# Optimization experiments

Hardware: AMD Instinct MI355X
Metric: run time of the kernel (lower is better)

The kernel has to match this reference:

```python
import jax, jax.numpy as jnp
import numpy as np
from jax import lax

B, T, D, H = 64, 256, 512, 1024  # batch, n_seq(time), seq_len(feat), hidden_dim

def _lstm(xs, h0, c0, W, U, b):
    # xs: (T, B, in_dim); W: (in_dim, 4H); U: (H, 4H); gate order i,f,g,o
    def step(carry, xt):
        h, c = carry
        gates = xt @ W + h @ U + b  # (B, 4H)
        i, f, g, o = jnp.split(gates, 4, axis=-1)
        c = jax.nn.sigmoid(f) * c + jax.nn.sigmoid(i) * jnp.tanh(g)
        h = jax.nn.sigmoid(o) * jnp.tanh(c)
        return (h, c), h
    (hT, cT), ys = lax.scan(step, (h0, c0), xs)
    return ys, (hT, cT)

def setup_inputs() -> dict:
    key = jax.random.key(0)
    ks = jax.random.split(key, 20)
    s = 0.02
    inp = {
        "x": jax.random.normal(ks[0], (B, T, D), jnp.float32),
        "h0": jax.random.normal(ks[1], (B, H), jnp.float32) * 0.1,
        "c0": jax.random.normal(ks[2], (B, H), jnp.float32) * 0.1,
        "W1": jax.random.normal(ks[3], (D, 4 * H), jnp.float32) * s,
        "U1": jax.random.normal(ks[4], (H, 4 * H), jnp.float32) * s,
        "b1": jnp.zeros((4 * H,), jnp.float32),
        "W2": jax.random.normal(ks[5], (H, 4 * H), jnp.float32) * s,
        "U2": jax.random.normal(ks[6], (H, 4 * H), jnp.float32) * s,
        "b2": jnp.zeros((4 * H,), jnp.float32),
        "fc1_w": jax.random.normal(ks[7], (H, H // 2), jnp.float32) * s,
        "fc1_b": jnp.zeros((H // 2,), jnp.float32),
        "fc2_w": jax.random.normal(ks[8], (H // 2 * T, 36), jnp.float32) * s,
        "fc2_b": jnp.zeros((36,), jnp.float32),
        "fc3_w": jax.random.normal(ks[9], (36, 6), jnp.float32) * s,
        "fc3_b": jnp.zeros((6,), jnp.float32),
        "fc4_w": jax.random.normal(ks[10], (6, 6), jnp.float32) * s,
        "fc4_b": jnp.zeros((6,), jnp.float32),
    }
    return inp

def reference(x, h0, c0, W1, U1, b1, W2, U2, b2,
              fc1_w, fc1_b, fc2_w, fc2_b, fc3_w, fc3_b, fc4_w, fc4_b):
    xs = jnp.transpose(x, (1, 0, 2))           # (T, B, D)
    ys1, (h1, c1) = _lstm(xs, h0, c0, W1, U1, b1)
    ys2, _ = _lstm(ys1, h1, c1, W2, U2, b2)    # lstm2 seeded with lstm1 final states
    y = jnp.transpose(ys2, (1, 0, 2))          # (B, T, H)
    y = y @ fc1_w + fc1_b                      # (B, T, H/2)
    y = y.reshape(y.shape[0], -1)              # (B, T*H/2)
    y = y @ fc2_w + fc2_b
    y = y @ fc3_w + fc3_b
    y = y @ fc4_w + fc4_b
    return jax.nn.relu(y)
```

## Files before the change

kernel.cpp:

```cpp
#include <hip/hip_runtime.h>


#define NT 256

typedef _Float16 f16x8 __attribute__((ext_vector_type(8)));
typedef _Float16 f16x4 __attribute__((ext_vector_type(4)));
typedef float f32x4 __attribute__((ext_vector_type(4)));
typedef unsigned long long u64;

__device__ __forceinline__ float sigm(float x)   { return 1.0f / (1.0f + __expf(-x)); }
__device__ __forceinline__ float tanh_f(float x) { return 1.0f - 2.0f / (__expf(2.0f * x) + 1.0f); }

__device__ __forceinline__ void barrier_lds() {
  asm volatile("s_waitcnt lgkmcnt(0)" ::: "memory");
  __builtin_amdgcn_s_barrier();
  asm volatile("" ::: "memory");
}


__global__ void prep_x_kernel(const float* __restrict__ x, _Float16* __restrict__ xh) {
  int id = blockIdx.x * blockDim.x + threadIdx.x;
  int j = id & 7, b = (id >> 3) & 63, cg = (id >> 9) & 63, t = id >> 15;
  xh[id] = (_Float16)x[((size_t)b * 256 + t) * 512 + cg * 8 + j];
}

__global__ void swizzle_b_kernel(const float* __restrict__ src0, const float* __restrict__ src1,
                                 int k0, int K, int N, int srcStride, int permute,
                                 _Float16* __restrict__ dst) {
  int id = blockIdx.x * blockDim.x + threadIdx.x;
  int total = (N / 16) * (K / 32) * 64;
  if (id >= total) return;
  int lane = id & 63;
  int kb = (id >> 6) % (K / 32);
  int nt = id / ((K / 32) * 64);
  int kbase = kb * 32 + ((lane >> 4) << 3);
  int pc = nt * 16 + (lane & 15);
  int oc = permute ? ((pc & 3) * 1024 + (pc >> 2)) : pc;
  f16x8 v;
  #pragma unroll
  for (int j = 0; j < 8; ++j) {
    int k = kbase + j;
    float f = (k < k0) ? src0[(size_t)k * srcStride + oc]
                       : src1[(size_t)(k - k0) * srcStride + oc];
    v[j] = (_Float16)f;
  }
  ((f16x8*)dst)[id] = v;
}

__global__ void prep_small_kernel(const float* __restrict__ b1, const float* __restrict__ b2,
                                  const float* __restrict__ h0,
                                  float* __restrict__ b1p, float* __restrict__ b2p,
                                  _Float16* __restrict__ ys1_0, int* __restrict__ bar) {
  int i = blockIdx.x * blockDim.x + threadIdx.x;
  if (i < 4096) {
    int oc = (i & 3) * 1024 + (i >> 2);
    b1p[i] = b1[oc];
    b2p[i] = b2[oc];
  }
  if (i < 65536) {
    int j = i & 7, b = (i >> 3) & 63, cg = i >> 9;
    ys1_0[i] = (_Float16)h0[b * 1024 + cg * 8 + j];
  }
  if (i < 16384) bar[i] = 0;
}

__global__ void sentinel_fill_kernel(_Float16* __restrict__ ys1, _Float16* __restrict__ ys2) {
  size_t i = (size_t)blockIdx.x * blockDim.x + threadIdx.x;
  uint4 s = {0x7FFF7FFFu, 0x7FFF7FFFu, 0x7FFF7FFFu, 0x7FFF7FFFu};
  ((uint4*)(ys1 + 65536))[i] = s;
  ((uint4*)(ys2 + 65536))[i] = s;
}

__launch_bounds__(256, 2)
__global__ void xg_gemm_kernel(const _Float16* __restrict__ xsrc, size_t xts, int kxb,
                               const _Float16* __restrict__ bfrag, const float* __restrict__ biasp,
                               _Float16* __restrict__ xg) {
  __shared__ _Float16 Bs[2 * 32 * 64 * 8];
  const int tid = threadIdx.x;
  const int lane = tid & 63;
  const int w = tid >> 6;
  const int btc = blockIdx.x >> 8;
  const int gb = blockIdx.x & 255;
  const int mb = gb & 1, nb = gb >> 1;
  const int KB = kxb + 32;
  if (tid == 0)
    (void)__hip_atomic_load((const int*)biasp, __ATOMIC_ACQUIRE, __HIP_MEMORY_SCOPE_AGENT);
  __syncthreads();
  #pragma unroll
  for (int h = 0; h < 2; ++h) {
    const uint4* s = (const uint4*)bfrag + (size_t)((2 * nb + h) * KB) * 64;
    uint4* d = (uint4*)Bs + h * 2048;
    for (int i = tid; i < kxb * 64; i += NT) d[i] = s[i];
  }
  __syncthreads();
  const f16x8* Bv = (const f16x8*)Bs;
  const int q = lane >> 4;
  const float bias0 = biasp[(2 * nb + 0) * 16 + (lane & 15)];
  const float bias1 = biasp[(2 * nb + 1) * 16 + (lane & 15)];
  for (int i = 0; i < 32; ++i) {
    int t = btc * 128 + i * 4 + w;
    const f16x8* ax = (const f16x8*)(xsrc + (size_t)t * xts);
    f32x4 acc[4];
    acc[0] = (f32x4){bias0, bias0, bias0, bias0};
    acc[1] = (f32x4){bias0, bias0, bias0, bias0};
    acc[2] = (f32x4){bias1, bias1, bias1, bias1};
    acc[3] = (f32x4){bias1, bias1, bias1, bias1};
    #pragma unroll 8
    for (int kb = 0; kb < kxb; ++kb) {
      f16x8 a0 = ax[(kb * 4 + q) * 64 + mb * 32 + (lane & 15)];
      f16x8 a1 = ax[(kb * 4 + q) * 64 + mb * 32 + 16 + (lane & 15)];
      f16x8 b0 = Bv[kb * 64 + lane];
      f16x8 b1v = Bv[2048 + kb * 64 + lane];
      acc[0] = __builtin_amdgcn_mfma_f32_16x16x32_f16(a0, b0, acc[0], 0, 0, 0);
      acc[1] = __builtin_amdgcn_mfma_f32_16x16x32_f16(a1, b0, acc[1], 0, 0, 0);
      acc[2] = __builtin_amdgcn_mfma_f32_16x16x32_f16(a0, b1v, acc[2], 0, 0, 0);
      acc[3] = __builtin_amdgcn_mfma_f32_16x16x32_f16(a1, b1v, acc[3], 0, 0, 0);
    }
    #pragma unroll
    for (int wp = 0; wp < 4; ++wp) {
      f16x4 hv;
      #pragma unroll
      for (int j = 0; j < 4; ++j) hv[j] = (_Float16)acc[wp][j];
      ((f16x4*)xg)[((size_t)t * 256 + gb) * 256 + wp * 64 + lane] = hv;
    }
  }
}

__launch_bounds__(NT, 1)
__global__ void lstm_layer_kernel(const _Float16* __restrict__ xg,
                                  _Float16* hseq, const _Float16* __restrict__ hinit,
                                  const _Float16* __restrict__ bfrag, int kxb,
                                  const float* __restrict__ cin, float* __restrict__ cout,
                                  int* bar) {
  __shared__ _Float16 Bs[2 * 32 * 64 * 8];
  __shared__ _Float16 As[128 * 32 * 8];
  __shared__ __align__(16) float gt[4][16 * 20];
  __shared__ u64 hl[4][16];
  const int tid = threadIdx.x;
  const int lane = tid & 63;
  const int w = tid >> 6;
  const int wm = w & 1, wn = w >> 1;
  const int blk = blockIdx.x;
  const int mb = blk & 1, nb = blk >> 1;
  const int KB = kxb + 32;

  if (tid == 0)
    (void)__hip_atomic_load(&bar[1024], __ATOMIC_ACQUIRE, __HIP_MEMORY_SCOPE_AGENT);
  __syncthreads();

  #pragma unroll
  for (int h = 0; h < 2; ++h) {
    const uint4* s = (const uint4*)bfrag + (size_t)((2 * nb + h) * KB + kxb) * 64;
    uint4* d = (uint4*)Bs + h * 2048;
    for (int i = tid; i < 2048; i += NT) d[i] = s[i];
  }
  __syncthreads();

  const f16x8* Bv = (const f16x8*)Bs;
  const f16x8* Af = (const f16x8*)As;
  u64* As64 = (u64*)As;
  const int q = lane >> 4;
  const int lrow = wm * 16 + (lane & 15);
  float cc = cin[(size_t)(mb * 32 + wm * 16 + (lane >> 2)) * 1024 + nb * 8 + wn * 4 + (lane & 3)];
  float* gw = &gt[w][0];
  _Float16* hw = (_Float16*)&hl[w][0];
  const u64 hstIdx = (u64)(nb * 128 + (mb * 32 + wm * 16 + (lane & 15)) * 2 + wn);
  int* fbase = bar + mb * 4096;
  const int* fpoll = fbase + (size_t)(w * 32 + (lane & 31)) * 32;
  int* fown = fbase + nb * 32;

  for (int t = 0; t < 256; ++t) {
    f16x4 xgv = ((const f16x4*)xg)[((size_t)t * 256 + blk) * 256 + w * 64 + lane];
    if (t) {
      for (;;) {
        int v = __hip_atomic_load(fpoll, __ATOMIC_RELAXED, __HIP_MEMORY_SCOPE_AGENT);
        if (__all(v >= t)) break;
        __builtin_amdgcn_s_sleep(1);
      }
      asm volatile("" ::: "memory");
    }
    const u64* hp = (const u64*)((t == 0) ? hinit : (hseq + (size_t)t * 65536))
                  + (size_t)(w * 32) * 128 + mb * 64 + lane;
    u64 hvv[32];
    #pragma unroll
    for (int i = 0; i < 32; ++i)
      hvv[i] = __hip_atomic_load(hp + (size_t)i * 128, __ATOMIC_RELAXED, __HIP_MEMORY_SCOPE_AGENT);
    for (;;) {
      unsigned np = 0;
      #pragma unroll
      for (int i = 0; i < 32; ++i)
        np |= (((unsigned)hvv[i] == 0x7FFF7FFFu) ? 1u : 0u) << i;
      if (__all(np == 0)) break;
      __builtin_amdgcn_s_sleep(1);
      #pragma unroll
      for (int i = 0; i < 32; ++i)
        if ((np >> i) & 1)
          hvv[i] = __hip_atomic_load(hp + (size_t)i * 128, __ATOMIC_RELAXED, __HIP_MEMORY_SCOPE_AGENT);
    }
    #pragma unroll
    for (int i = 0; i < 32; ++i) As64[(w * 32 + i) * 64 + lane] = hvv[i];
    barrier_lds();
    f32x4 acc = {(float)xgv[0], (float)xgv[1], (float)xgv[2], (float)xgv[3]};
    f32x4 acc2 = {0.f, 0.f, 0.f, 0.f};
    #pragma unroll 8
    for (int kb = 0; kb < 16; ++kb) {
      acc  = __builtin_amdgcn_mfma_f32_16x16x32_f16(Af[((2 * kb) * 4 + q) * 32 + lrow],
                                                    Bv[(wn * 32 + 2 * kb) * 64 + lane], acc, 0, 0, 0);
      acc2 = __builtin_amdgcn_mfma_f32_16x16x32_f16(Af[((2 * kb + 1) * 4 + q) * 32 + lrow],
                                                    Bv[(wn * 32 + 2 * kb + 1) * 64 + lane], acc2, 0, 0, 0);
    }
    #pragma unroll
    for (int r = 0; r < 4; ++r) acc[r] += acc2[r];
    #pragma unroll
    for (int r = 0; r < 4; ++r) gw[(q * 4 + r) * 20 + (lane & 15)] = acc[r];
    float4 gv = *(float4*)&gw[(lane >> 2) * 20 + (lane & 3) * 4];
    cc = sigm(gv.y) * cc + sigm(gv.x) * tanh_f(gv.z);
    float hn = sigm(gv.w) * tanh_f(cc);
    hw[lane] = (_Float16)hn;
    u64 hv = hl[w][lane & 15];
    if (lane < 16)
      __hip_atomic_store((u64*)(hseq + (size_t)(t + 1) * 65536) + hstIdx, hv,
                         __ATOMIC_RELAXED, __HIP_MEMORY_SCOPE_AGENT);
    barrier_lds();
    if (t < 255 && tid == 0)
      __hip_atomic_store(fown, t + 1, __ATOMIC_RELAXED, __HIP_MEMORY_SCOPE_AGENT);
  }
  if (cout)
    cout[(size_t)(mb * 32 + wm * 16 + (lane >> 2)) * 1024 + nb * 8 + wn * 4 + (lane & 3)] = cc;
}


__launch_bounds__(256, 1)
__global__ void fc1_gemm_kernel(const _Float16* __restrict__ ys2, const _Float16* __restrict__ wfrag,
                                const float* __restrict__ fc1b, float* __restrict__ Y1) {
  const int mb = blockIdx.x >> 3;
  const int nb = blockIdx.x & 7;
  const int tid = threadIdx.x;
  const int lane = tid & 63;
  const int w = tid >> 6;
  const int q = lane >> 4;
  const int R0 = mb * 64 + w * 16;
  const int arow = R0 + (lane & 15);
  const int u = arow >> 6;
  const int b = arow & 63;
  const f16x8* A = (const f16x8*)(ys2 + (size_t)(u + 1) * 65536);
  const f16x8* W = (const f16x8*)wfrag;
  f32x4 acc[4];
  #pragma unroll
  for (int n = 0; n < 4; ++n) acc[n] = (f32x4){0.f, 0.f, 0.f, 0.f};
  #pragma unroll 4
  for (int kb = 0; kb < 32; ++kb) {
    f16x8 a = A[(kb * 4 + q) * 64 + b];
    #pragma unroll
    for (int n = 0; n < 4; ++n)
      acc[n] = __builtin_amdgcn_mfma_f32_16x16x32_f16(a, W[(((nb * 4 + n) * 32) + kb) * 64 + lane],
                                                      acc[n], 0, 0, 0);
  }
  const int rb = R0 + (q << 2);
  #pragma unroll
  for (int n = 0; n < 4; ++n) {
    int col = nb * 64 + n * 16 + (lane & 15);
    float bias = fc1b[col];
    #pragma unroll
    for (int r = 0; r < 4; ++r) {
      int R = rb + r;
      Y1[((size_t)(R & 63) * 256 + (R >> 6)) * 512 + col] = acc[n][r] + bias;
    }
  }
}

__global__ void fc2_partial_kernel(const float* __restrict__ Y1, const float* __restrict__ fc2w,
                                   float* __restrict__ part) {
  int kc = blockIdx.x;
  int tid = threadIdx.x;
  int b = tid >> 2, qq = tid & 3;
  const float* y = Y1 + (size_t)b * 131072 + (size_t)kc * 512;
  const float* wbase = fc2w + (size_t)kc * 512 * 36 + qq * 9;
  float acc[9];
  #pragma unroll
  for (int j = 0; j < 9; ++j) acc[j] = 0.f;
  for (int k = 0; k < 512; ++k) {
    float yv = y[k];
    const float* wr = wbase + (size_t)k * 36;
    #pragma unroll
    for (int j = 0; j < 9; ++j) acc[j] = fmaf(yv, wr[j], acc[j]);
  }
  float* o = part + ((size_t)kc * 64 + b) * 36 + qq * 9;
  #pragma unroll
  for (int j = 0; j < 9; ++j) o[j] = acc[j];
}

__global__ void fc_final_kernel(const float* __restrict__ part, const float* __restrict__ fc2b,
                                const float* __restrict__ fc3w, const float* __restrict__ fc3b,
                                const float* __restrict__ fc4w, const float* __restrict__ fc4b,
                                float* __restrict__ out) {
  __shared__ float z2[64 * 36];
  __shared__ float z3[64 * 6];
  int tid = threadIdx.x;
  for (int idx = tid; idx < 64 * 36; idx += 384) {
    int b = idx / 36, m = idx % 36;
    float s = fc2b[m];
    for (int kc = 0; kc < 256; ++kc) s += part[((size_t)kc * 64 + b) * 36 + m];
    z2[idx] = s;
  }
  __syncthreads();
  {
    int b = tid / 6, n = tid % 6;
    float s = fc3b[n];
    #pragma unroll 4
    for (int m = 0; m < 36; ++m) s += z2[b * 36 + m] * fc3w[m * 6 + n];
    z3[tid] = s;
  }
  __syncthreads();
  {
    int b = tid / 6, n = tid % 6;
    float s = fc4b[n];
    #pragma unroll
    for (int m = 0; m < 6; ++m) s += z3[b * 6 + m] * fc4w[m * 6 + n];
    out[tid] = fmaxf(s, 0.0f);
  }
}


extern "C" void kernel_launch(void* const* d_in, const int* in_sizes, int n_in,
                              void* d_out, int out_size, void* d_ws, size_t ws_size,
                              hipStream_t stream) {
  const float* x    = (const float*)d_in[0];
  const float* h0   = (const float*)d_in[1];
  const float* c0   = (const float*)d_in[2];
  const float* W1   = (const float*)d_in[3];
  const float* U1   = (const float*)d_in[4];
  const float* b1   = (const float*)d_in[5];
  const float* W2   = (const float*)d_in[6];
  const float* U2   = (const float*)d_in[7];
  const float* b2   = (const float*)d_in[8];
  const float* fc1w = (const float*)d_in[9];
  const float* fc1b = (const float*)d_in[10];
  const float* fc2w = (const float*)d_in[11];
  const float* fc2b = (const float*)d_in[12];
  const float* fc3w = (const float*)d_in[13];
  const float* fc3b = (const float*)d_in[14];
  const float* fc4w = (const float*)d_in[15];
  const float* fc4b = (const float*)d_in[16];
  float* out = (float*)d_out;

  char* p = (char*)d_ws;
  auto alloc = [&](size_t bytes) { char* r = p; p += (bytes + 255) & ~(size_t)255; return r; };
  _Float16* xh    = (_Float16*)alloc(8388608ull * 2);
  _Float16* wu1f  = (_Float16*)alloc(1536ull * 4096 * 2);
  _Float16* wu2f  = (_Float16*)alloc(2048ull * 4096 * 2);
  _Float16* fc1wf = (_Float16*)alloc(1024ull * 512 * 2);
  float* b1p      = (float*)alloc(4096 * 4);
  float* b2p      = (float*)alloc(4096 * 4);
  _Float16* ys1   = (_Float16*)alloc(257ull * 65536 * 2);
  _Float16* ys2   = (_Float16*)alloc(257ull * 65536 * 2);
  float* cfin     = (float*)alloc(65536 * 4);
  _Float16* xg    = (_Float16*)alloc(256ull * 65536 * 4 * 2);
  float* part     = (float*)alloc(256ull * 64 * 36 * 4);
  int* bar        = (int*)alloc(16384 * 4);
  float* Y1       = (float*)xg;
  (void)in_sizes; (void)n_in; (void)out_size; (void)ws_size;

  prep_x_kernel<<<8388608 / 256, 256, 0, stream>>>(x, xh);
  swizzle_b_kernel<<<(256 * 48 * 64) / 256, 256, 0, stream>>>(W1, U1, 512, 1536, 4096, 4096, 1, wu1f);
  swizzle_b_kernel<<<(256 * 64 * 64) / 256, 256, 0, stream>>>(W2, U2, 1024, 2048, 4096, 4096, 1, wu2f);
  swizzle_b_kernel<<<(32 * 32 * 64) / 256, 256, 0, stream>>>(fc1w, fc1w, 1024, 1024, 512, 512, 0, fc1wf);
  prep_small_kernel<<<256, 256, 0, stream>>>(b1, b2, h0, b1p, b2p, ys1, bar);
  sentinel_fill_kernel<<<8192, 256, 0, stream>>>(ys1, ys2);

  xg_gemm_kernel<<<512, 256, 0, stream>>>(xh, (size_t)32768, 16, wu1f, b1p, xg);
  lstm_layer_kernel<<<256, NT, 0, stream>>>(xg, ys1, ys1, wu1f, 16, c0, cfin, bar);
  xg_gemm_kernel<<<512, 256, 0, stream>>>(ys1 + 65536, (size_t)65536, 32, wu2f, b2p, xg);
  lstm_layer_kernel<<<256, NT, 0, stream>>>(xg, ys2, ys1 + (size_t)256 * 65536, wu2f, 32,
                                            cfin, nullptr, bar + 8192);

  fc1_gemm_kernel<<<2048, 256, 0, stream>>>(ys2, fc1wf, fc1b, Y1);
  fc2_partial_kernel<<<256, 256, 0, stream>>>(Y1, fc2w, part);
  fc_final_kernel<<<1, 384, 0, stream>>>(part, fc2b, fc3w, fc3b, fc4w, fc4b, out);
}
```

Baseline: 3.011 ms.

## Halve LSTM grid with 512-thread blocks and pipeline h-state loads in chunks

The recurrent LSTM kernel now runs 128 blocks of 512 threads, each owning twice as many hidden columns, so fewer blocks take part in the per-step flag synchronisation. Instead of loading the whole previous h into LDS before the MFMAs start, it loads h in four K-chunks and overlaps the global load of the next chunk with MFMA on the current one, using extra barriers. The fc2 reduction also moves out of the single-block final kernel into a small parallel kernel. The added barriers per step and the larger blocks are the costs, and the flag indexing was rewritten to match the new block mapping.

```diff
diff --git a/kernel.cpp b/kernel.cpp
--- a/kernel.cpp
+++ b/kernel.cpp
@@ -1,7 +1,7 @@
 #include <hip/hip_runtime.h>
 
 
-#define NT 256
+#define NT 512
 
 typedef _Float16 f16x8 __attribute__((ext_vector_type(8)));
 typedef _Float16 f16x4 __attribute__((ext_vector_type(4)));
@@ -90,7 +90,7 @@
   for (int h = 0; h < 2; ++h) {
     const uint4* s = (const uint4*)bfrag + (size_t)((2 * nb + h) * KB) * 64;
     uint4* d = (uint4*)Bs + h * 2048;
-    for (int i = tid; i < kxb * 64; i += NT) d[i] = s[i];
+    for (int i = tid; i < kxb * 64; i += 256) d[i] = s[i];
   }
   __syncthreads();
   const f16x8* Bv = (const f16x8*)Bs;
@@ -132,16 +132,15 @@
                                   const _Float16* __restrict__ bfrag, int kxb,
                                   const float* __restrict__ cin, float* __restrict__ cout,
                                   int* bar) {
-  __shared__ _Float16 Bs[2 * 32 * 64 * 8];
-  __shared__ _Float16 As[128 * 32 * 8];
-  __shared__ __align__(16) float gt[4][16 * 20];
-  __shared__ u64 hl[4][16];
+  __shared__ _Float16 Bs[4 * 32 * 64 * 8];
+  __shared__ _Float16 As[32 * 32 * 8];
+  __shared__ __align__(16) float gt[8][16 * 20];
+  __shared__ u64 hl[8][16];
   const int tid = threadIdx.x;
   const int lane = tid & 63;
   const int w = tid >> 6;
   const int wm = w & 1, wn = w >> 1;
-  const int blk = blockIdx.x;
-  const int mb = blk & 1, nb = blk >> 1;
+  const int mb = blockIdx.x & 1, nb2 = blockIdx.x >> 1;
   const int KB = kxb + 32;
 
   if (tid == 0)
@@ -149,8 +148,8 @@
   __syncthreads();
 
   #pragma unroll
-  for (int h = 0; h < 2; ++h) {
-    const uint4* s = (const uint4*)bfrag + (size_t)((2 * nb + h) * KB + kxb) * 64;
+  for (int h = 0; h < 4; ++h) {
+    const uint4* s = (const uint4*)bfrag + (size_t)((4 * nb2 + h) * KB + kxb) * 64;
     uint4* d = (uint4*)Bs + h * 2048;
     for (int i = tid; i < 2048; i += NT) d[i] = s[i];
   }
@@ -161,16 +160,22 @@
   u64* As64 = (u64*)As;
   const int q = lane >> 4;
   const int lrow = wm * 16 + (lane & 15);
-  float cc = cin[(size_t)(mb * 32 + wm * 16 + (lane >> 2)) * 1024 + nb * 8 + wn * 4 + (lane & 3)];
+  float cc = cin[(size_t)(mb * 32 + wm * 16 + (lane >> 2)) * 1024
+                 + nb2 * 16 + wn * 4 + (lane & 3)];
   float* gw = &gt[w][0];
   _Float16* hw = (_Float16*)&hl[w][0];
-  const u64 hstIdx = (u64)(nb * 128 + (mb * 32 + wm * 16 + (lane & 15)) * 2 + wn);
-  int* fbase = bar + mb * 4096;
-  const int* fpoll = fbase + (size_t)(w * 32 + (lane & 31)) * 32;
-  int* fown = fbase + nb * 32;
-
+  const u64 hstIdx = (u64)((2 * nb2 + (wn >> 1)) * 128
+                           + (mb * 32 + wm * 16 + (lane & 15)) * 2 + (wn & 1));
+  const int* fpoll = bar + (size_t)(mb * 64 + lane) * 32;
+  int* fown = bar + (size_t)(mb * 64 + nb2) * 32;
+  const int gbm = ((2 * nb2 + (wn >> 1)) << 1) | mb;
+  const int wq = wm + 2 * (wn & 1);
+  const size_t xgBase = (size_t)gbm * 256 + wq * 64 + lane;
+
+  u64 pre[4];
   for (int t = 0; t < 256; ++t) {
-    f16x4 xgv = ((const f16x4*)xg)[((size_t)t * 256 + blk) * 256 + w * 64 + lane];
+    f16x4 xgv = ((const f16x4*)xg)[(size_t)t * 65536 + xgBase];
+    const u64* Sg = (const u64*)((t == 0) ? hinit : (hseq + (size_t)t * 65536));
     if (t) {
       for (;;) {
         int v = __hip_atomic_load(fpoll, __ATOMIC_RELAXED, __HIP_MEMORY_SCOPE_AGENT);
@@ -179,35 +184,65 @@
       }
       asm volatile("" ::: "memory");
     }
-    const u64* hp = (const u64*)((t == 0) ? hinit : (hseq + (size_t)t * 65536))
-                  + (size_t)(w * 32) * 128 + mb * 64 + lane;
-    u64 hvv[32];
-    #pragma unroll
-    for (int i = 0; i < 32; ++i)
-      hvv[i] = __hip_atomic_load(hp + (size_t)i * 128, __ATOMIC_RELAXED, __HIP_MEMORY_SCOPE_AGENT);
-    for (;;) {
-      unsigned np = 0;
+    {
+      const u64* src = Sg + (size_t)(w * 4) * 128 + mb * 64 + lane;
       #pragma unroll
-      for (int i = 0; i < 32; ++i)
-        np |= (((unsigned)hvv[i] == 0x7FFF7FFFu) ? 1u : 0u) << i;
-      if (__all(np == 0)) break;
-      __builtin_amdgcn_s_sleep(1);
+      for (int i = 0; i < 4; ++i)
+        pre[i] = __hip_atomic_load(src + (size_t)i * 128, __ATOMIC_RELAXED, __HIP_MEMORY_SCOPE_AGENT);
+      for (;;) {
+        unsigned np = 0;
+        #pragma unroll
+        for (int i = 0; i < 4; ++i)
+          np |= (((unsigned)pre[i] == 0x7FFF7FFFu) ? 1u : 0u) << i;
+        if (__all(np == 0)) break;
+        __builtin_amdgcn_s_sleep(1);
+        #pragma unroll
+        for (int i = 0; i < 4; ++i)
+          if ((np >> i) & 1)
+            pre[i] = __hip_atomic_load(src + (size_t)i * 128, __ATOMIC_RELAXED, __HIP_MEMORY_SCOPE_AGENT);
+      }
       #pragma unroll
-      for (int i = 0; i < 32; ++i)
-        if ((np >> i) & 1)
-          hvv[i] = __hip_atomic_load(hp + (size_t)i * 128, __ATOMIC_RELAXED, __HIP_MEMORY_SCOPE_AGENT);
-    }
-    #pragma unroll
-    for (int i = 0; i < 32; ++i) As64[(w * 32 + i) * 64 + lane] = hvv[i];
+      for (int i = 0; i < 4; ++i) As64[(w * 4 + i) * 64 + lane] = pre[i];
+    }
     barrier_lds();
     f32x4 acc = {(float)xgv[0], (float)xgv[1], (float)xgv[2], (float)xgv[3]};
     f32x4 acc2 = {0.f, 0.f, 0.f, 0.f};
-    #pragma unroll 8
-    for (int kb = 0; kb < 16; ++kb) {
-      acc  = __builtin_amdgcn_mfma_f32_16x16x32_f16(Af[((2 * kb) * 4 + q) * 32 + lrow],
-                                                    Bv[(wn * 32 + 2 * kb) * 64 + lane], acc, 0, 0, 0);
-      acc2 = __builtin_amdgcn_mfma_f32_16x16x32_f16(Af[((2 * kb + 1) * 4 + q) * 32 + lrow],
-                                                    Bv[(wn * 32 + 2 * kb + 1) * 64 + lane], acc2, 0, 0, 0);
+    #pragma unroll
+    for (int p = 0; p < 4; ++p) {
+      if (p < 3) {
+        const u64* src = Sg + (size_t)((p + 1) * 32 + w * 4) * 128 + mb * 64 + lane;
+        #pragma unroll
+        for (int i = 0; i < 4; ++i)
+          pre[i] = __hip_atomic_load(src + (size_t)i * 128, __ATOMIC_RELAXED, __HIP_MEMORY_SCOPE_AGENT);
+      }
+      #pragma unroll
+      for (int j = 0; j < 8; j += 2) {
+        acc  = __builtin_amdgcn_mfma_f32_16x16x32_f16(Af[(4 * j + q) * 32 + lrow],
+                                                      Bv[(wn * 32 + 8 * p + j) * 64 + lane],
+                                                      acc, 0, 0, 0);
+        acc2 = __builtin_amdgcn_mfma_f32_16x16x32_f16(Af[(4 * j + 4 + q) * 32 + lrow],
+                                                      Bv[(wn * 32 + 8 * p + j + 1) * 64 + lane],
+                                                      acc2, 0, 0, 0);
+      }
+      barrier_lds();
+      if (p < 3) {
+        const u64* src = Sg + (size_t)((p + 1) * 32 + w * 4) * 128 + mb * 64 + lane;
+        for (;;) {
+          unsigned np = 0;
+          #pragma unroll
+          for (int i = 0; i < 4; ++i)
+            np |= (((unsigned)pre[i] == 0x7FFF7FFFu) ? 1u : 0u) << i;
+          if (__all(np == 0)) break;
+          __builtin_amdgcn_s_sleep(1);
+          #pragma unroll
+          for (int i = 0; i < 4; ++i)
+            if ((np >> i) & 1)
+              pre[i] = __hip_atomic_load(src + (size_t)i * 128, __ATOMIC_RELAXED, __HIP_MEMORY_SCOPE_AGENT);
+        }
+        #pragma unroll
+        for (int i = 0; i < 4; ++i) As64[(w * 4 + i) * 64 + lane] = pre[i];
+        barrier_lds();
+      }
     }
     #pragma unroll
     for (int r = 0; r < 4; ++r) acc[r] += acc2[r];
@@ -221,12 +256,12 @@
     if (lane < 16)
       __hip_atomic_store((u64*)(hseq + (size_t)(t + 1) * 65536) + hstIdx, hv,
                          __ATOMIC_RELAXED, __HIP_MEMORY_SCOPE_AGENT);
-    barrier_lds();
     if (t < 255 && tid == 0)
       __hip_atomic_store(fown, t + 1, __ATOMIC_RELAXED, __HIP_MEMORY_SCOPE_AGENT);
   }
   if (cout)
-    cout[(size_t)(mb * 32 + wm * 16 + (lane >> 2)) * 1024 + nb * 8 + wn * 4 + (lane & 3)] = cc;
+    cout[(size_t)(mb * 32 + wm * 16 + (lane >> 2)) * 1024
+         + nb2 * 16 + wn * 4 + (lane & 3)] = cc;
 }
 
 
@@ -290,19 +325,24 @@
   for (int j = 0; j < 9; ++j) o[j] = acc[j];
 }
 
-__global__ void fc_final_kernel(const float* __restrict__ part, const float* __restrict__ fc2b,
+__global__ void fc2_reduce_kernel(const float* __restrict__ part, const float* __restrict__ fc2b,
+                                  float* __restrict__ z2g) {
+  int idx = blockIdx.x * blockDim.x + threadIdx.x;
+  if (idx >= 2304) return;
+  int b = idx / 36, m = idx % 36;
+  float s = fc2b[m];
+  for (int kc = 0; kc < 256; ++kc) s += part[((size_t)kc * 64 + b) * 36 + m];
+  z2g[idx] = s;
+}
+
+__global__ void fc_final_kernel(const float* __restrict__ z2g,
                                 const float* __restrict__ fc3w, const float* __restrict__ fc3b,
                                 const float* __restrict__ fc4w, const float* __restrict__ fc4b,
                                 float* __restrict__ out) {
   __shared__ float z2[64 * 36];
   __shared__ float z3[64 * 6];
   int tid = threadIdx.x;
-  for (int idx = tid; idx < 64 * 36; idx += 384) {
-    int b = idx / 36, m = idx % 36;
-    float s = fc2b[m];
-    for (int kc = 0; kc < 256; ++kc) s += part[((size_t)kc * 64 + b) * 36 + m];
-    z2[idx] = s;
-  }
+  for (int idx = tid; idx < 64 * 36; idx += 384) z2[idx] = z2g[idx];
   __syncthreads();
   {
     int b = tid / 6, n = tid % 6;
@@ -358,6 +398,7 @@
   _Float16* xg    = (_Float16*)alloc(256ull * 65536 * 4 * 2);
   float* part     = (float*)alloc(256ull * 64 * 36 * 4);
   int* bar        = (int*)alloc(16384 * 4);
+  float* z2g      = (float*)alloc(2304 * 4);
   float* Y1       = (float*)xg;
   (void)in_sizes; (void)n_in; (void)out_size; (void)ws_size;
 
@@ -369,12 +410,13 @@
   sentinel_fill_kernel<<<8192, 256, 0, stream>>>(ys1, ys2);
 
   xg_gemm_kernel<<<512, 256, 0, stream>>>(xh, (size_t)32768, 16, wu1f, b1p, xg);
-  lstm_layer_kernel<<<256, NT, 0, stream>>>(xg, ys1, ys1, wu1f, 16, c0, cfin, bar);
+  lstm_layer_kernel<<<128, NT, 0, stream>>>(xg, ys1, ys1, wu1f, 16, c0, cfin, bar);
   xg_gemm_kernel<<<512, 256, 0, stream>>>(ys1 + 65536, (size_t)65536, 32, wu2f, b2p, xg);
-  lstm_layer_kernel<<<256, NT, 0, stream>>>(xg, ys2, ys1 + (size_t)256 * 65536, wu2f, 32,
+  lstm_layer_kernel<<<128, NT, 0, stream>>>(xg, ys2, ys1 + (size_t)256 * 65536, wu2f, 32,
                                             cfin, nullptr, bar + 8192);
 
   fc1_gemm_kernel<<<2048, 256, 0, stream>>>(ys2, fc1wf, fc1b, Y1);
   fc2_partial_kernel<<<256, 256, 0, stream>>>(Y1, fc2w, part);
-  fc_final_kernel<<<1, 384, 0, stream>>>(part, fc2b, fc3w, fc3b, fc4w, fc4b, out);
-}
+  fc2_reduce_kernel<<<9, 256, 0, stream>>>(part, fc2b, z2g);
+  fc_final_kernel<<<1, 384, 0, stream>>>(z2g, fc3w, fc3b, fc4w, fc4b, out);
+}
```

Measured after the change: 3.146 ms. 1.04x slower.
